# Performance work log

Hardware: AMD Instinct MI355X
Metric: run time of the kernel (lower is better)

The kernel has to match this reference:

```python
import jax, jax.numpy as jnp
import numpy as np

DIM = 16      # memory_columns = dim
HEADS = 2
ROWS = 2 * HEADS * DIM          # memory_rows = 64
COLS = DIM                      # 16
PREC = 16                       # memory_precision
MC = ROWS * COLS * PREC         # memory_cell_amount = 16384
EMB = 64                        # embedding_size
RH = 2                          # read_heads
OUT = ROWS * COLS               # output_size = memory_size = 1024
UNITS = OUT + 2 * ROWS + 2 * COLS  # controller LSTM units = 1184
DSTEPS = 2                      # discretization_steps

# standard sinusoidal positional encoding over ROWS+1 positions
_L = ROWS + 1
_pos = np.arange(_L, dtype=np.float32)[:, None]
_i = np.arange(EMB)[None, :]
_ang = _pos / np.power(10000.0, (2 * (_i // 2)) / EMB)
PE = jnp.asarray(np.where(_i % 2 == 0, np.sin(_ang), np.cos(_ang)).astype(np.float32))[None]  # (1, 65, 64)

# non-trainable (default) conductance ODE constants, stacked per synapse type:
# [input, recurrent, inhibitory, leakage]
COND = jnp.array([0.07915332, 1.0334609, 1.3365093, 0.4505964], jnp.float32)
MEAN = jnp.array([0.5, 0.07879465, 0.06618887, 0.0], jnp.float32)
STD = jnp.array([100.0, 100.0, 100.0, 1.0], jnp.float32)
TGT = jnp.array([1.5931877, 1.4378392, 0.0, 0.0], jnp.float32)
PART_STEP = jnp.float32(1.5573331 / DSTEPS)  # step_size / discretization_steps (capacitance = 1)


def _forward(queries, values, Wi, bi, Wm, bm, Wq, bq, Wk, bk, Wv, bv, Wo, bo, Wx, bl):
    B, Q, _ = queries.shape
    V = values.shape[1]
    dq = jnp.repeat(queries[:, :, None, :], V, 2)          # (B,Q,V,dim)
    dv = jnp.repeat(values[:, None, :, :], Q, 1)           # (B,Q,V,dim)
    mli = jnp.concatenate([dq, dv], -1).reshape(B * Q, V, 2 * DIM)  # (128,V,32)
    xs = jnp.swapaxes(mli, 0, 1)                           # (V,128,32) time-major
    BQ = B * Q                                             # == 128 (hardcoded in source)
    pot0 = jnp.broadcast_to(jnp.array([0.0, 1.0], jnp.float32), (BQ, MC, 2))
    scale = 1.0 / jnp.sqrt(jnp.float32(EMB))               # MHA key_dim = EMB

    def step(pot, x_t):
        # read memory row contents (even-indexed state entries = potentials)
        mem = pot[..., 0].reshape(BQ, ROWS, COLS * PREC)   # (128,64,256)
        emb_mem = mem @ Wm + bm                            # (128,64,64)
        emb_in = (x_t @ Wi + bi)[:, None, :]               # (128,1,64)
        aug = jnp.concatenate([emb_in, emb_mem], 1) + PE   # (128,65,64)
        # multi-head self-attention; only the row-0 query is kept downstream
        q = jnp.einsum('bd,dhk->bhk', aug[:, 0], Wq) + bq
        k = jnp.einsum('bld,dhk->blhk', aug, Wk) + bk
        v = jnp.einsum('bld,dhk->blhk', aug, Wv) + bv
        attn = jax.nn.softmax(jnp.einsum('bhk,blhk->bhl', q, k) * scale, -1)
        ctx = jnp.einsum('bhl,blhk->bhk', attn, v)
        o = jnp.einsum('bhk,hkd->bd', ctx, Wo) + bo        # (128,64)
        # LSTM controller over a length-1 sequence with zero initial state:
        # recurrent term h0 @ Wr vanishes, so z = x @ Wx + b
        z = o @ Wx + bl                                    # (128,4*1184)
        zi, zf, zg, zo = jnp.split(z, 4, -1)
        c = jax.nn.sigmoid(zi) * jnp.tanh(zg)
        h = jax.nn.sigmoid(zo) * jnp.tanh(c)
        out = h[:, :OUT]                                   # (128,1024)
        # multi-step Euler integration of the conductance ODE
        inp = jnp.zeros_like(pot)                          # neuron_inputs = zeros
        p = pot
        for _ in range(DSTEPS):
            pre = jnp.stack([inp, p, p[..., ::-1], jnp.full_like(p, jnp.inf)], -1)  # (128,MC,2,4)
            sig = jax.nn.sigmoid(STD * (pre - MEAN))
            curr = COND * sig * (TGT - p[..., None])
            p = p + jnp.sum(curr, -1) * PART_STEP
        return p, out

    _, ys = jax.lax.scan(step, pot0, xs)
    # keras RNN default: last-step output; then reshape as in MemoryLayerAttention.call
    return ys[-1].reshape(-1, Q, DIM)                      # (512,16,16)


def setup_inputs():
    key = jax.random.key(0)
    ks = jax.random.split(key, 10)
    n = lambda k, s: jax.random.normal(k, s, jnp.float32) * 0.05
    return {
        'queries': jax.random.normal(ks[0], (8, 16, DIM), jnp.float32),
        'values': jax.random.normal(ks[1], (8, 8, DIM), jnp.float32),
        'Wi': n(ks[2], (2 * DIM, EMB)), 'bi': jnp.zeros((EMB,), jnp.float32),
        'Wm': n(ks[3], (COLS * PREC, EMB)), 'bm': jnp.zeros((EMB,), jnp.float32),
        'Wq': n(ks[4], (EMB, RH, EMB)), 'bq': jnp.zeros((RH, EMB), jnp.float32),
        'Wk': n(ks[5], (EMB, RH, EMB)), 'bk': jnp.zeros((RH, EMB), jnp.float32),
        'Wv': n(ks[6], (EMB, RH, EMB)), 'bv': jnp.zeros((RH, EMB), jnp.float32),
        'Wo': n(ks[7], (RH, EMB, EMB)), 'bo': jnp.zeros((EMB,), jnp.float32),
        'Wx': n(ks[8], (EMB, 4 * UNITS)), 'bl': jnp.zeros((4 * UNITS,), jnp.float32),
    }


def reference(queries, values, Wi, bi, Wm, bm, Wq, bq, Wk, bk, Wv, bv, Wo, bo, Wx, bl):
    return _forward(queries, values, Wi, bi, Wm, bm, Wq, bq, Wk, bk, Wv, bv, Wo, bo, Wx, bl)
```

## Files before the change

kernel.cpp:

```cpp
#include <hip/hip_runtime.h>
#include <math.h>

#define EMB 64
#define UNITS 1184
#define OUTN 1024
#define ZCOLS 4736

__device__ __align__(16) float g_kv[16384];

__device__ __forceinline__ float stable_sigmoid(float x) {
    const float e = expf(-fabsf(x));
    const float r = 1.0f / (1.0f + e);
    return (x >= 0.0f) ? r : 1.0f - r;
}

__device__ __forceinline__ float pot_sub(float pc, float po) {
    float t0 = 0.07915332f * stable_sigmoid(100.0f * (0.0f - 0.5f))        * (1.5931877f - pc);
    float t1 = 1.0334609f  * stable_sigmoid(100.0f * (pc - 0.07879465f))   * (1.4378392f - pc);
    float t2 = 1.3365093f  * stable_sigmoid(100.0f * (po - 0.06618887f))   * (0.0f - pc);
    float t3 = 0.4505964f  * 1.0f                                          * (0.0f - pc);
    return pc + (t0 + t1 + t2 + t3) * (1.5573331f / 2.0f);
}

__device__ __forceinline__ float pot_a7() {
    float p0 = 0.0f, p1 = 1.0f;
    for (int t = 0; t < 7; ++t)
        for (int s = 0; s < 2; ++s) {
            float n0 = pot_sub(p0, p1);
            float n1 = pot_sub(p1, p0);
            p0 = n0; p1 = n1;
        }
    return p0;
}

__global__ __launch_bounds__(256)
void precompute_kv(const float* __restrict__ Wm, const float* __restrict__ bm,
                   const float* __restrict__ Wk, const float* __restrict__ bk,
                   const float* __restrict__ Wv, const float* __restrict__ bv,
                   float* __restrict__ sink) {
    __shared__ float part[4][EMB];
    __shared__ float s_m[EMB];
    __shared__ __align__(16) float aug[2][EMB];
    const int tid = threadIdx.x;

    const int idx = blockIdx.x * 256 + tid;
    const int isv = idx >> 13;
    const float* Wrole = isv ? Wv : Wk;
    const float pf = Wrole[tid * 32];

    const int rg = tid >> 6, c = tid & 63;
    float wm[64];
    #pragma unroll
    for (int r = 0; r < 64; ++r) wm[r] = Wm[(rg * 64 + r) * EMB + c];
    const float a = pot_a7();
    float s = 0.0f;
    #pragma unroll
    for (int r = 0; r < 64; ++r) s += wm[r];
    part[rg][c] = s;
    if (pf == -1.2345678e38f) sink[0] = pf;
    __syncthreads();
    if (tid < EMB) {
        s_m[tid] = a * (part[0][tid] + part[1][tid] + part[2][tid] + part[3][tid]) + bm[tid];
    }
    __syncthreads();

    const int l0 = (blockIdx.x & 31) * 2;
    if (tid < 128) {
        const int l = tid >> 6, d = tid & 63;
        const float inv = exp2f(-(float)(2 * (d >> 1)) * (13.287712379549449f / 64.0f));
        const float ang = (float)(l0 + l + 1) * inv;
        const float pe  = (d & 1) ? cosf(ang) : sinf(ang);
        aug[l][d] = s_m[d] + pe;
    }
    __syncthreads();

    const int r = idx & 8191;
    const int l = (r >> 7) - l0;
    const int t = r & 127;
    const float* bb = isv ? bv : bk;

    float w[64];
    #pragma unroll
    for (int d = 0; d < 64; ++d) w[d] = Wrole[d * 128 + t];
    float av[64];
    const float4* a4 = (const float4*)aug[l];
    #pragma unroll
    for (int d4 = 0; d4 < 16; ++d4) {
        const float4 q = a4[d4];
        av[4 * d4 + 0] = q.x; av[4 * d4 + 1] = q.y;
        av[4 * d4 + 2] = q.z; av[4 * d4 + 3] = q.w;
    }
    float sv = bb[t];
    #pragma unroll
    for (int d = 0; d < 64; ++d) sv += av[d] * w[d];
    g_kv[idx] = sv;
}

__global__ __launch_bounds__(256)
void attend_out(const float* __restrict__ queries, const float* __restrict__ values,
                const float* __restrict__ Wi, const float* __restrict__ bi,
                const float* __restrict__ Wq, const float* __restrict__ bq,
                const float* __restrict__ Wk, const float* __restrict__ bk,
                const float* __restrict__ Wv, const float* __restrict__ bv,
                const float* __restrict__ Wo, const float* __restrict__ bo,
                const float* __restrict__ Wx, const float* __restrict__ bl,
                float* __restrict__ out) {
    const int b = blockIdx.x >> 2, tid = threadIdx.x;
    const int j0 = (blockIdx.x & 3) << 8;
    const int j  = j0 | tid;
    __shared__ __align__(16) float e[EMB];
    __shared__ __align__(16) float qv[128];
    __shared__ __align__(16) float k0[128];
    __shared__ __align__(16) float v0[128];
    __shared__ __align__(16) float ctx[128];
    __shared__ __align__(16) float o[EMB];
    __shared__ __align__(16) float att[2][68];

    float pf = 0.0f;
    {
        #pragma unroll
        for (int kk = 0; kk < 6; ++kk) {
            const int li = tid * 6 + kk;
            const int z  = li >> 9;
            const int r  = (li >> 3) & 63;
            const int cc = (li & 7) << 5;
            const int zoff = (z == 0) ? 0 : ((z == 1) ? 2 * UNITS : 3 * UNITS);
            pf += Wx[r * ZCOLS + zoff + j0 + cc];
        }
        pf += Wq[tid * 32];
        pf += Wk[tid * 32];
        pf += Wv[tid * 32];
        pf += Wo[tid * 32];
        if (tid < 64) pf += Wi[tid * 32];
        pf += g_kv[tid * 32];
        pf += g_kv[8192 + tid * 32];
    }
    float zi = bl[j], zg = bl[2 * UNITS + j], zo = bl[3 * UNITS + j];

    if (tid < EMB) {
        float xr[32], wi[32];
        const float* qp = queries + b * 16;
        const float* vp = values + (b >> 4) * 128 + 112;
        #pragma unroll
        for (int i = 0; i < 16; ++i) xr[i] = qp[i];
        #pragma unroll
        for (int i = 0; i < 16; ++i) xr[16 + i] = vp[i];
        #pragma unroll
        for (int i = 0; i < 32; ++i) wi[i] = Wi[i * EMB + tid];
        float s = bi[tid] + ((tid & 1) ? 1.0f : 0.0f);
        #pragma unroll
        for (int i = 0; i < 32; ++i) s += xr[i] * wi[i];
        e[tid] = s;
    }
    if (pf == -1.2345678e38f) out[j] = pf;
    __syncthreads();

    float ev[64];
    {
        const float4* e4 = (const float4*)e;
        #pragma unroll
        for (int d4 = 0; d4 < 16; ++d4) {
            const float4 q = e4[d4];
            ev[4 * d4 + 0] = q.x; ev[4 * d4 + 1] = q.y;
            ev[4 * d4 + 2] = q.z; ev[4 * d4 + 3] = q.w;
        }
    }
    if (tid < 128) {
        float w[64];
        #pragma unroll
        for (int d = 0; d < 64; ++d) w[d] = Wq[d * 128 + tid];
        float s = bq[tid];
        #pragma unroll
        for (int d = 0; d < 64; ++d) s += ev[d] * w[d];
        qv[tid] = s;
        #pragma unroll
        for (int d = 0; d < 64; ++d) w[d] = Wv[d * 128 + tid];
        float sv = bv[tid];
        #pragma unroll
        for (int d = 0; d < 64; ++d) sv += ev[d] * w[d];
        v0[tid] = sv;
    } else {
        const int t = tid - 128;
        float w[64];
        #pragma unroll
        for (int d = 0; d < 64; ++d) w[d] = Wk[d * 128 + t];
        float s = bk[t];
        #pragma unroll
        for (int d = 0; d < 64; ++d) s += ev[d] * w[d];
        k0[t] = s;
    }
    __syncthreads();

    if (tid < 128) {
        const int h = tid >> 6, p = tid & 63;
        float qh[64], kr[64];
        {
            const float4* q4 = (const float4*)(qv + h * 64);
            #pragma unroll
            for (int d4 = 0; d4 < 16; ++d4) {
                const float4 q = q4[d4];
                qh[4 * d4 + 0] = q.x; qh[4 * d4 + 1] = q.y;
                qh[4 * d4 + 2] = q.z; qh[4 * d4 + 3] = q.w;
            }
        }
        if (p == 0) {
            const float4* k4 = (const float4*)(k0 + h * 64);
            #pragma unroll
            for (int d4 = 0; d4 < 16; ++d4) {
                const float4 q = k4[d4];
                kr[4 * d4 + 0] = q.x; kr[4 * d4 + 1] = q.y;
                kr[4 * d4 + 2] = q.z; kr[4 * d4 + 3] = q.w;
            }
        } else {
            const float4* k4 = (const float4*)(g_kv + (p - 1) * 128 + h * 64);
            #pragma unroll
            for (int d4 = 0; d4 < 16; ++d4) {
                const float4 q = k4[d4];
                kr[4 * d4 + 0] = q.x; kr[4 * d4 + 1] = q.y;
                kr[4 * d4 + 2] = q.z; kr[4 * d4 + 3] = q.w;
            }
        }
        float s = 0.0f;
        #pragma unroll
        for (int d = 0; d < 64; ++d) s += qh[d] * kr[d];
        s *= 0.125f;
        float s64 = -1e30f;
        if (p == 63) {
            const float4* k4 = (const float4*)(g_kv + 63 * 128 + h * 64);
            #pragma unroll
            for (int d4 = 0; d4 < 16; ++d4) {
                const float4 q = k4[d4];
                kr[4 * d4 + 0] = q.x; kr[4 * d4 + 1] = q.y;
                kr[4 * d4 + 2] = q.z; kr[4 * d4 + 3] = q.w;
            }
            float t64 = 0.0f;
            #pragma unroll
            for (int d = 0; d < 64; ++d) t64 += qh[d] * kr[d];
            s64 = t64 * 0.125f;
        }
        s64 = __shfl(s64, 63, 64);
        float m = s;
        #pragma unroll
        for (int mask = 1; mask < 64; mask <<= 1) m = fmaxf(m, __shfl_xor(m, mask, 64));
        m = fmaxf(m, s64);
        const float ex  = expf(s - m);
        const float e64 = expf(s64 - m);
        float sum = ex;
        #pragma unroll
        for (int mask = 1; mask < 64; mask <<= 1) sum += __shfl_xor(sum, mask, 64);
        sum += e64;
        const float inv = 1.0f / sum;
        att[h][p] = ex * inv;
        if (p == 63) att[h][64] = e64 * inv;
    }
    __syncthreads();

    if (tid < 128) {
        const int h = tid >> 6;
        float av[65];
        {
            const float4* a4 = (const float4*)att[h];
            #pragma unroll
            for (int d4 = 0; d4 < 16; ++d4) {
                const float4 q = a4[d4];
                av[4 * d4 + 0] = q.x; av[4 * d4 + 1] = q.y;
                av[4 * d4 + 2] = q.z; av[4 * d4 + 3] = q.w;
            }
            av[64] = att[h][64];
        }
        float vr[64];
        const float* vm = g_kv + 8192 + tid;
        #pragma unroll
        for (int l = 0; l < 64; ++l) vr[l] = vm[l * 128];
        float s = av[0] * v0[tid];
        #pragma unroll
        for (int l = 0; l < 64; ++l) s += av[l + 1] * vr[l];
        ctx[tid] = s;
    }
    __syncthreads();

    if (tid < 64) {
        float s = bo[tid];
        float cx[64], wo[64];
        const float4* c4 = (const float4*)ctx;
        #pragma unroll
        for (int t4 = 0; t4 < 16; ++t4) {
            const float4 q = c4[t4];
            cx[4 * t4 + 0] = q.x; cx[4 * t4 + 1] = q.y;
            cx[4 * t4 + 2] = q.z; cx[4 * t4 + 3] = q.w;
        }
        #pragma unroll
        for (int t = 0; t < 64; ++t) wo[t] = Wo[t * 64 + tid];
        #pragma unroll
        for (int t = 0; t < 64; ++t) s += cx[t] * wo[t];
        #pragma unroll
        for (int t4 = 0; t4 < 16; ++t4) {
            const float4 q = c4[16 + t4];
            cx[4 * t4 + 0] = q.x; cx[4 * t4 + 1] = q.y;
            cx[4 * t4 + 2] = q.z; cx[4 * t4 + 3] = q.w;
        }
        #pragma unroll
        for (int t = 0; t < 64; ++t) wo[t] = Wo[(64 + t) * 64 + tid];
        #pragma unroll
        for (int t = 0; t < 64; ++t) s += cx[t] * wo[t];
        o[tid] = s;
    }
    __syncthreads();

    float ov[64];
    {
        const float4* o4 = (const float4*)o;
        #pragma unroll
        for (int d4 = 0; d4 < 16; ++d4) {
            const float4 q = o4[d4];
            ov[4 * d4 + 0] = q.x; ov[4 * d4 + 1] = q.y;
            ov[4 * d4 + 2] = q.z; ov[4 * d4 + 3] = q.w;
        }
    }
    const float* col = Wx + j;
    #pragma unroll
    for (int d = 0; d < 64; ++d) {
        const float* row = col + d * ZCOLS;
        zi += ov[d] * row[0];
        zg += ov[d] * row[2 * UNITS];
        zo += ov[d] * row[3 * UNITS];
    }
    const float c = stable_sigmoid(zi) * tanhf(zg);
    out[b * OUTN + j] = stable_sigmoid(zo) * tanhf(c);
}

extern "C" void kernel_launch(void* const* d_in, const int* in_sizes, int n_in,
                              void* d_out, int out_size, void* d_ws, size_t ws_size,
                              hipStream_t stream) {
    const float* queries = (const float*)d_in[0];
    const float* values  = (const float*)d_in[1];
    const float* Wi = (const float*)d_in[2];
    const float* bi = (const float*)d_in[3];
    const float* Wm = (const float*)d_in[4];
    const float* bm = (const float*)d_in[5];
    const float* Wq = (const float*)d_in[6];
    const float* bq = (const float*)d_in[7];
    const float* Wk = (const float*)d_in[8];
    const float* bk = (const float*)d_in[9];
    const float* Wv = (const float*)d_in[10];
    const float* bv = (const float*)d_in[11];
    const float* Wo = (const float*)d_in[12];
    const float* bo = (const float*)d_in[13];
    const float* Wx = (const float*)d_in[14];
    const float* bl = (const float*)d_in[15];
    float* out = (float*)d_out;
    (void)d_ws; (void)ws_size;

    precompute_kv<<<64, 256, 0, stream>>>(Wm, bm, Wk, bk, Wv, bv, out);
    attend_out<<<512, 256, 0, stream>>>(queries, values, Wi, bi, Wq, bq, Wk, bk,
                                        Wv, bv, Wo, bo, Wx, bl, out);
}
```

Before: 110.9 us.

## Run attention chain in a single wavefront and drop intermediate block barriers

The embed, Q/K/V projection, softmax, context and output projection stages now all run inside one 64-lane wavefront, so four block-wide __syncthreads between them go away. The other three wavefronts only prefetch the Wx, Wq and Wo rows into cache while the first wave works. The cost is that one wave does several times more serial FMA and memory work (six projections instead of one or two per thread), which lengthens the critical path. Shared-memory visibility inside a single wave is assumed rather than enforced by a barrier.

```diff
diff --git a/kernel.cpp b/kernel.cpp
--- a/kernel.cpp
+++ b/kernel.cpp
@@ -95,6 +95,17 @@
     for (int d = 0; d < 64; ++d) sv += av[d] * w[d];
     g_kv[idx] = sv;
 }
+
+#define STAGE64(dst, srcptr)                                         \
+    {                                                                \
+        const float4* _s4 = (const float4*)(srcptr);                 \
+        _Pragma("unroll")                                            \
+        for (int _d4 = 0; _d4 < 16; ++_d4) {                         \
+            const float4 _q = _s4[_d4];                              \
+            dst[4 * _d4 + 0] = _q.x; dst[4 * _d4 + 1] = _q.y;        \
+            dst[4 * _d4 + 2] = _q.z; dst[4 * _d4 + 3] = _q.w;        \
+        }                                                            \
+    }
 
 __global__ __launch_bounds__(256)
 void attend_out(const float* __restrict__ queries, const float* __restrict__ values,
@@ -116,207 +127,196 @@
     __shared__ __align__(16) float o[EMB];
     __shared__ __align__(16) float att[2][68];
 
+    float zi = bl[j], zg = bl[2 * UNITS + j], zo = bl[3 * UNITS + j];
+
     float pf = 0.0f;
-    {
+    if (tid >= 64) {
+        const int t = tid - 64;
         #pragma unroll
-        for (int kk = 0; kk < 6; ++kk) {
-            const int li = tid * 6 + kk;
+        for (int kk = 0; kk < 8; ++kk) {
+            const int li = t * 8 + kk;
             const int z  = li >> 9;
             const int r  = (li >> 3) & 63;
             const int cc = (li & 7) << 5;
             const int zoff = (z == 0) ? 0 : ((z == 1) ? 2 * UNITS : 3 * UNITS);
             pf += Wx[r * ZCOLS + zoff + j0 + cc];
         }
-        pf += Wq[tid * 32];
-        pf += Wk[tid * 32];
-        pf += Wv[tid * 32];
-        pf += Wo[tid * 32];
-        if (tid < 64) pf += Wi[tid * 32];
-        pf += g_kv[tid * 32];
-        pf += g_kv[8192 + tid * 32];
-    }
-    float zi = bl[j], zg = bl[2 * UNITS + j], zo = bl[3 * UNITS + j];
-
-    if (tid < EMB) {
-        float xr[32], wi[32];
-        const float* qp = queries + b * 16;
-        const float* vp = values + (b >> 4) * 128 + 112;
-        #pragma unroll
-        for (int i = 0; i < 16; ++i) xr[i] = qp[i];
-        #pragma unroll
-        for (int i = 0; i < 16; ++i) xr[16 + i] = vp[i];
-        #pragma unroll
-        for (int i = 0; i < 32; ++i) wi[i] = Wi[i * EMB + tid];
-        float s = bi[tid] + ((tid & 1) ? 1.0f : 0.0f);
-        #pragma unroll
-        for (int i = 0; i < 32; ++i) s += xr[i] * wi[i];
-        e[tid] = s;
-    }
+        if (t < 128) {
+            pf += Wq[t * 64] + Wq[t * 64 + 32];
+        } else {
+            const int u = t - 128;
+            pf += Wo[u * 128] + Wo[u * 128 + 32] + Wo[u * 128 + 64] + Wo[u * 128 + 96];
+        }
+        if (t < 64) pf += Wi[t * 32];
+    } else {
+        const int lane = tid;
+
+        {
+            float xr[32], wi[32];
+            const float* qp = queries + b * 16;
+            const float* vp = values + (b >> 4) * 128 + 112;
+            #pragma unroll
+            for (int i = 0; i < 16; ++i) xr[i] = qp[i];
+            #pragma unroll
+            for (int i = 0; i < 16; ++i) xr[16 + i] = vp[i];
+            #pragma unroll
+            for (int i = 0; i < 32; ++i) wi[i] = Wi[i * EMB + lane];
+            float s = bi[lane] + ((lane & 1) ? 1.0f : 0.0f);
+            #pragma unroll
+            for (int i = 0; i < 32; ++i) s += xr[i] * wi[i];
+            e[lane] = s;
+        }
+
+        {
+            float ev[64];
+            STAGE64(ev, e);
+            float w[64];
+            #pragma unroll
+            for (int d = 0; d < 64; ++d) w[d] = Wq[d * 128 + lane];
+            float s = bq[lane];
+            #pragma unroll
+            for (int d = 0; d < 64; ++d) s += ev[d] * w[d];
+            qv[lane] = s;
+            #pragma unroll
+            for (int d = 0; d < 64; ++d) w[d] = Wq[d * 128 + 64 + lane];
+            s = bq[64 + lane];
+            #pragma unroll
+            for (int d = 0; d < 64; ++d) s += ev[d] * w[d];
+            qv[64 + lane] = s;
+            #pragma unroll
+            for (int d = 0; d < 64; ++d) w[d] = Wk[d * 128 + lane];
+            s = bk[lane];
+            #pragma unroll
+            for (int d = 0; d < 64; ++d) s += ev[d] * w[d];
+            k0[lane] = s;
+            #pragma unroll
+            for (int d = 0; d < 64; ++d) w[d] = Wk[d * 128 + 64 + lane];
+            s = bk[64 + lane];
+            #pragma unroll
+            for (int d = 0; d < 64; ++d) s += ev[d] * w[d];
+            k0[64 + lane] = s;
+            #pragma unroll
+            for (int d = 0; d < 64; ++d) w[d] = Wv[d * 128 + lane];
+            s = bv[lane];
+            #pragma unroll
+            for (int d = 0; d < 64; ++d) s += ev[d] * w[d];
+            v0[lane] = s;
+            #pragma unroll
+            for (int d = 0; d < 64; ++d) w[d] = Wv[d * 128 + 64 + lane];
+            s = bv[64 + lane];
+            #pragma unroll
+            for (int d = 0; d < 64; ++d) s += ev[d] * w[d];
+            v0[64 + lane] = s;
+        }
+
+        const int p = lane;
+        float s0, s1, x0 = -1e30f, x1 = -1e30f;
+        {
+            float qh[64], kr[64];
+            STAGE64(qh, qv);
+            if (p == 0) { STAGE64(kr, k0); }
+            else        { STAGE64(kr, g_kv + (p - 1) * 128); }
+            float s = 0.0f;
+            #pragma unroll
+            for (int d = 0; d < 64; ++d) s += qh[d] * kr[d];
+            s0 = s * 0.125f;
+            if (p == 63) {
+                STAGE64(kr, g_kv + 63 * 128);
+                float t64 = 0.0f;
+                #pragma unroll
+                for (int d = 0; d < 64; ++d) t64 += qh[d] * kr[d];
+                x0 = t64 * 0.125f;
+            }
+            STAGE64(qh, qv + 64);
+            if (p == 0) { STAGE64(kr, k0 + 64); }
+            else        { STAGE64(kr, g_kv + (p - 1) * 128 + 64); }
+            s = 0.0f;
+            #pragma unroll
+            for (int d = 0; d < 64; ++d) s += qh[d] * kr[d];
+            s1 = s * 0.125f;
+            if (p == 63) {
+                STAGE64(kr, g_kv + 63 * 128 + 64);
+                float t64 = 0.0f;
+                #pragma unroll
+                for (int d = 0; d < 64; ++d) t64 += qh[d] * kr[d];
+                x1 = t64 * 0.125f;
+            }
+        }
+        {
+            const float b0 = __shfl(x0, 63, 64);
+            float m = s0;
+            #pragma unroll
+            for (int mask = 1; mask < 64; mask <<= 1) m = fmaxf(m, __shfl_xor(m, mask, 64));
+            m = fmaxf(m, b0);
+            const float ex  = expf(s0 - m);
+            const float e64 = expf(b0 - m);
+            float sum = ex;
+            #pragma unroll
+            for (int mask = 1; mask < 64; mask <<= 1) sum += __shfl_xor(sum, mask, 64);
+            sum += e64;
+            const float inv = 1.0f / sum;
+            att[0][p] = ex * inv;
+            if (p == 63) att[0][64] = e64 * inv;
+        }
+        {
+            const float b1 = __shfl(x1, 63, 64);
+            float m = s1;
+            #pragma unroll
+            for (int mask = 1; mask < 64; mask <<= 1) m = fmaxf(m, __shfl_xor(m, mask, 64));
+            m = fmaxf(m, b1);
+            const float ex  = expf(s1 - m);
+            const float e64 = expf(b1 - m);
+            float sum = ex;
+            #pragma unroll
+            for (int mask = 1; mask < 64; mask <<= 1) sum += __shfl_xor(sum, mask, 64);
+            sum += e64;
+            const float inv = 1.0f / sum;
+            att[1][p] = ex * inv;
+            if (p == 63) att[1][64] = e64 * inv;
+        }
+
+        {
+            float av[65], vr[64];
+            STAGE64(av, att[0]);
+            av[64] = att[0][64];
+            #pragma unroll
+            for (int l = 0; l < 64; ++l) vr[l] = g_kv[8192 + l * 128 + lane];
+            float s = av[0] * v0[lane];
+            #pragma unroll
+            for (int l = 0; l < 64; ++l) s += av[l + 1] * vr[l];
+            ctx[lane] = s;
+            STAGE64(av, att[1]);
+            av[64] = att[1][64];
+            #pragma unroll
+            for (int l = 0; l < 64; ++l) vr[l] = g_kv[8192 + l * 128 + 64 + lane];
+            s = av[0] * v0[64 + lane];
+            #pragma unroll
+            for (int l = 0; l < 64; ++l) s += av[l + 1] * vr[l];
+            ctx[64 + lane] = s;
+        }
+
+        {
+            float cx[64], wo[64];
+            STAGE64(cx, ctx);
+            #pragma unroll
+            for (int t = 0; t < 64; ++t) wo[t] = Wo[t * 64 + lane];
+            float s = bo[lane];
+            #pragma unroll
+            for (int t = 0; t < 64; ++t) s += cx[t] * wo[t];
+            STAGE64(cx, ctx + 64);
+            #pragma unroll
+            for (int t = 0; t < 64; ++t) wo[t] = Wo[(64 + t) * 64 + lane];
+            #pragma unroll
+            for (int t = 0; t < 64; ++t) s += cx[t] * wo[t];
+            o[lane] = s;
+        }
+    }
+
     if (pf == -1.2345678e38f) out[j] = pf;
     __syncthreads();
 
-    float ev[64];
-    {
-        const float4* e4 = (const float4*)e;
-        #pragma unroll
-        for (int d4 = 0; d4 < 16; ++d4) {
-            const float4 q = e4[d4];
-            ev[4 * d4 + 0] = q.x; ev[4 * d4 + 1] = q.y;
-            ev[4 * d4 + 2] = q.z; ev[4 * d4 + 3] = q.w;
-        }
-    }
-    if (tid < 128) {
-        float w[64];
-        #pragma unroll
-        for (int d = 0; d < 64; ++d) w[d] = Wq[d * 128 + tid];
-        float s = bq[tid];
-        #pragma unroll
-        for (int d = 0; d < 64; ++d) s += ev[d] * w[d];
-        qv[tid] = s;
-        #pragma unroll
-        for (int d = 0; d < 64; ++d) w[d] = Wv[d * 128 + tid];
-        float sv = bv[tid];
-        #pragma unroll
-        for (int d = 0; d < 64; ++d) sv += ev[d] * w[d];
-        v0[tid] = sv;
-    } else {
-        const int t = tid - 128;
-        float w[64];
-        #pragma unroll
-        for (int d = 0; d < 64; ++d) w[d] = Wk[d * 128 + t];
-        float s = bk[t];
-        #pragma unroll
-        for (int d = 0; d < 64; ++d) s += ev[d] * w[d];
-        k0[t] = s;
-    }
-    __syncthreads();
-
-    if (tid < 128) {
-        const int h = tid >> 6, p = tid & 63;
-        float qh[64], kr[64];
-        {
-            const float4* q4 = (const float4*)(qv + h * 64);
-            #pragma unroll
-            for (int d4 = 0; d4 < 16; ++d4) {
-                const float4 q = q4[d4];
-                qh[4 * d4 + 0] = q.x; qh[4 * d4 + 1] = q.y;
-                qh[4 * d4 + 2] = q.z; qh[4 * d4 + 3] = q.w;
-            }
-        }
-        if (p == 0) {
-            const float4* k4 = (const float4*)(k0 + h * 64);
-            #pragma unroll
-            for (int d4 = 0; d4 < 16; ++d4) {
-                const float4 q = k4[d4];
-                kr[4 * d4 + 0] = q.x; kr[4 * d4 + 1] = q.y;
-                kr[4 * d4 + 2] = q.z; kr[4 * d4 + 3] = q.w;
-            }
-        } else {
-            const float4* k4 = (const float4*)(g_kv + (p - 1) * 128 + h * 64);
-            #pragma unroll
-            for (int d4 = 0; d4 < 16; ++d4) {
-                const float4 q = k4[d4];
-                kr[4 * d4 + 0] = q.x; kr[4 * d4 + 1] = q.y;
-                kr[4 * d4 + 2] = q.z; kr[4 * d4 + 3] = q.w;
-            }
-        }
-        float s = 0.0f;
-        #pragma unroll
-        for (int d = 0; d < 64; ++d) s += qh[d] * kr[d];
-        s *= 0.125f;
-        float s64 = -1e30f;
-        if (p == 63) {
-            const float4* k4 = (const float4*)(g_kv + 63 * 128 + h * 64);
-            #pragma unroll
-            for (int d4 = 0; d4 < 16; ++d4) {
-                const float4 q = k4[d4];
-                kr[4 * d4 + 0] = q.x; kr[4 * d4 + 1] = q.y;
-                kr[4 * d4 + 2] = q.z; kr[4 * d4 + 3] = q.w;
-            }
-            float t64 = 0.0f;
-            #pragma unroll
-            for (int d = 0; d < 64; ++d) t64 += qh[d] * kr[d];
-            s64 = t64 * 0.125f;
-        }
-        s64 = __shfl(s64, 63, 64);
-        float m = s;
-        #pragma unroll
-        for (int mask = 1; mask < 64; mask <<= 1) m = fmaxf(m, __shfl_xor(m, mask, 64));
-        m = fmaxf(m, s64);
-        const float ex  = expf(s - m);
-        const float e64 = expf(s64 - m);
-        float sum = ex;
-        #pragma unroll
-        for (int mask = 1; mask < 64; mask <<= 1) sum += __shfl_xor(sum, mask, 64);
-        sum += e64;
-        const float inv = 1.0f / sum;
-        att[h][p] = ex * inv;
-        if (p == 63) att[h][64] = e64 * inv;
-    }
-    __syncthreads();
-
-    if (tid < 128) {
-        const int h = tid >> 6;
-        float av[65];
-        {
-            const float4* a4 = (const float4*)att[h];
-            #pragma unroll
-            for (int d4 = 0; d4 < 16; ++d4) {
-                const float4 q = a4[d4];
-                av[4 * d4 + 0] = q.x; av[4 * d4 + 1] = q.y;
-                av[4 * d4 + 2] = q.z; av[4 * d4 + 3] = q.w;
-            }
-            av[64] = att[h][64];
-        }
-        float vr[64];
-        const float* vm = g_kv + 8192 + tid;
-        #pragma unroll
-        for (int l = 0; l < 64; ++l) vr[l] = vm[l * 128];
-        float s = av[0] * v0[tid];
-        #pragma unroll
-        for (int l = 0; l < 64; ++l) s += av[l + 1] * vr[l];
-        ctx[tid] = s;
-    }
-    __syncthreads();
-
-    if (tid < 64) {
-        float s = bo[tid];
-        float cx[64], wo[64];
-        const float4* c4 = (const float4*)ctx;
-        #pragma unroll
-        for (int t4 = 0; t4 < 16; ++t4) {
-            const float4 q = c4[t4];
-            cx[4 * t4 + 0] = q.x; cx[4 * t4 + 1] = q.y;
-            cx[4 * t4 + 2] = q.z; cx[4 * t4 + 3] = q.w;
-        }
-        #pragma unroll
-        for (int t = 0; t < 64; ++t) wo[t] = Wo[t * 64 + tid];
-        #pragma unroll
-        for (int t = 0; t < 64; ++t) s += cx[t] * wo[t];
-        #pragma unroll
-        for (int t4 = 0; t4 < 16; ++t4) {
-            const float4 q = c4[16 + t4];
-            cx[4 * t4 + 0] = q.x; cx[4 * t4 + 1] = q.y;
-            cx[4 * t4 + 2] = q.z; cx[4 * t4 + 3] = q.w;
-        }
-        #pragma unroll
-        for (int t = 0; t < 64; ++t) wo[t] = Wo[(64 + t) * 64 + tid];
-        #pragma unroll
-        for (int t = 0; t < 64; ++t) s += cx[t] * wo[t];
-        o[tid] = s;
-    }
-    __syncthreads();
-
     float ov[64];
-    {
-        const float4* o4 = (const float4*)o;
-        #pragma unroll
-        for (int d4 = 0; d4 < 16; ++d4) {
-            const float4 q = o4[d4];
-            ov[4 * d4 + 0] = q.x; ov[4 * d4 + 1] = q.y;
-            ov[4 * d4 + 2] = q.z; ov[4 * d4 + 3] = q.w;
-        }
-    }
+    STAGE64(ov, o);
     const float* col = Wx + j;
     #pragma unroll
     for (int d = 0; d < 64; ++d) {
```

Result: slower. 121.2 us (+9.3%).
